# Optimization experiments

Measured on AMD Instinct MI355X. Metric: run time of the kernel, lower is better.

The kernel has to match this reference:

```python
import jax, jax.numpy as jnp
import numpy as np

N, D, E = 50000, 128, 100000
H1, H2, H3 = 8, 8, 4
NEG_SLOPE = 0.2  # PyG GATv2Conv default negative_slope


def _gatv2_layer(x, src, dst, Wl, Wr, att, b, heads):
    # GATv2Conv(in=D, out=D, heads=heads, concat=False), share_weights=False
    C = Wl.shape[1] // heads
    xl = (x @ Wl).reshape(-1, heads, C)  # source-side transform (x_j)
    xr = (x @ Wr).reshape(-1, heads, C)  # target-side transform (x_i)
    m = jax.nn.leaky_relu(xl[src] + xr[dst], NEG_SLOPE)      # [E,H,C]
    e = jnp.einsum('ehc,hc->eh', m, att)                      # [E,H]
    # segment softmax over incoming edges of each destination node
    emax = jax.ops.segment_max(e, dst, num_segments=N)        # [N,H]
    a = jnp.exp(e - emax[dst])
    denom = jax.ops.segment_sum(a, dst, num_segments=N)       # [N,H] (>0: self-loops)
    a = a / denom[dst]
    out = jax.ops.segment_sum(xl[src] * a[:, :, None], dst, num_segments=N)  # [N,H,C]
    return out.mean(axis=1) + b  # concat=False -> head mean, then bias


def setup_inputs() -> dict:
    key = jax.random.key(0)
    ks = jax.random.split(key, 16)
    x = jax.random.normal(ks[0], (N, D), dtype=jnp.float32)
    src = jax.random.randint(ks[1], (E,), 0, N)
    dst = jax.random.randint(ks[2], (E,), 0, N)
    src = jnp.where(src == dst, (src + 1) % N, src)  # no pre-existing self loops
    edge_index = jnp.stack([src, dst]).astype(jnp.int64)
    s = 1.0 / np.sqrt(D)
    def lin(k, h):
        return jax.random.uniform(k, (D, h * D), jnp.float32, -s, s)
    def attn(k, h):
        return jax.random.uniform(k, (h, D), jnp.float32, -s, s)
    return {
        'x': x, 'edge_index': edge_index,
        'W1l': lin(ks[3], H1), 'W1r': lin(ks[4], H1), 'att1': attn(ks[5], H1), 'b1': jnp.zeros((D,), jnp.float32),
        'W2l': lin(ks[6], H2), 'W2r': lin(ks[7], H2), 'att2': attn(ks[8], H2), 'b2': jnp.zeros((D,), jnp.float32),
        'W3l': lin(ks[9], H3), 'W3r': lin(ks[10], H3), 'att3': attn(ks[11], H3), 'b3': jnp.zeros((D,), jnp.float32),
    }


def reference(x, edge_index, W1l, W1r, att1, b1, W2l, W2r, att2, b2, W3l, W3r, att3, b3):
    # PyG GATv2Conv adds self loops by default
    loops = jnp.arange(N, dtype=edge_index.dtype)
    src = jnp.concatenate([edge_index[0], loops])
    dst = jnp.concatenate([edge_index[1], loops])
    h = x + _gatv2_layer(x, src, dst, W1l, W1r, att1, b1, H1)
    h = jax.nn.elu(h)  # dropout is identity in eval mode
    h = h + _gatv2_layer(h, src, dst, W2l, W2r, att2, b2, H2)
    h = jax.nn.elu(h)
    h = h + _gatv2_layer(h, src, dst, W3l, W3r, att3, b3, H3)
    return h
```

## Files before the change

### kernel.cpp

```cpp
#include <hip/hip_runtime.h>

#define NN 50000
#define DD 128
#define EE 100000
#define ET (EE + NN)

typedef __attribute__((ext_vector_type(4))) float f32x4;
typedef __attribute__((ext_vector_type(2))) float f32x2;
typedef __attribute__((ext_vector_type(8))) short bf16x8;
typedef __attribute__((ext_vector_type(4))) unsigned short u16x4;
typedef __attribute__((ext_vector_type(4))) unsigned int u32x4;

static __device__ __forceinline__ unsigned short f2bf(float f) {
  union { float f; unsigned int u; } v; v.f = f;
  unsigned int r = (v.u + 0x7FFFu + ((v.u >> 16) & 1u)) >> 16;
  return (unsigned short)r;
}
static __device__ __forceinline__ float bflo(unsigned int u) {
  union { unsigned int u; float f; } v; v.u = u << 16; return v.f;
}
static __device__ __forceinline__ float bfhi(unsigned int u) {
  union { unsigned int u; float f; } v; v.u = u & 0xffff0000u; return v.f;
}

__global__ void k_count(const int* __restrict__ ei, int* __restrict__ counts) {
  int i = blockIdx.x * blockDim.x + threadIdx.x;
  if (i >= ET) return;
  int dst = (i < EE) ? ei[EE + i] : (i - EE);
  if (dst < 0 || dst >= NN) return;
  atomicAdd(&counts[dst], 1);
}

__global__ __launch_bounds__(1024) void k_scan(const int* __restrict__ counts,
                                               int* __restrict__ offs,
                                               int* __restrict__ cursor) {
  __shared__ int buf[1024];
  const int tid = threadIdx.x;
  int carry = 0;
  for (int base = 0; base < NN; base += 4096) {
    int i0 = base + tid * 4;
    int v[4];
#pragma unroll
    for (int q = 0; q < 4; ++q) { int i = i0 + q; v[q] = (i < NN) ? counts[i] : 0; }
    int s = v[0] + v[1] + v[2] + v[3];
    buf[tid] = s;
    __syncthreads();
    for (int off = 1; off < 1024; off <<= 1) {
      int t = (tid >= off) ? buf[tid - off] : 0;
      __syncthreads();
      buf[tid] += t;
      __syncthreads();
    }
    int excl = carry + buf[tid] - s;
    int tot = buf[1023];
#pragma unroll
    for (int q = 0; q < 4; ++q) {
      int i = i0 + q;
      if (i < NN) { offs[i] = excl; cursor[i] = excl; }
      excl += v[q];
    }
    carry += tot;
    __syncthreads();
  }
  if (tid == 0) offs[NN] = carry;
}

__global__ void k_fill(const int* __restrict__ ei, int* __restrict__ cursor,
                       int* __restrict__ srcs) {
  int i = blockIdx.x * blockDim.x + threadIdx.x;
  if (i >= ET) return;
  int src, dst;
  if (i < EE) { src = ei[i]; dst = ei[EE + i]; }
  else { src = dst = i - EE; }
  if (dst < 0 || dst >= NN) return;
  if (src < 0 || src >= NN) src = dst;
  int pos = atomicAdd(&cursor[dst], 1);
  if (pos >= 0 && pos < ET) srcs[pos] = src;
}

__global__ void k_wT(const float* __restrict__ W, unsigned short* __restrict__ WT, int Nout) {
  int i = blockIdx.x * blockDim.x + threadIdx.x;
  int total = Nout * DD;
  if (i >= total) return;
  int n = i >> 7, k = i & 127;
  WT[i] = f2bf(W[(size_t)k * Nout + n]);
}

__global__ void k_cvt(const float* __restrict__ in, unsigned short* __restrict__ out, int total4) {
  int i = blockIdx.x * blockDim.x + threadIdx.x;
  if (i >= total4) return;
  f32x4 v = *(const f32x4*)(in + (size_t)i * 4);
  u16x4 w;
  w.x = f2bf(v.x); w.y = f2bf(v.y); w.z = f2bf(v.z); w.w = f2bf(v.w);
  *(u16x4*)(out + (size_t)i * 4) = w;
}

__global__ void k_atts(const float* __restrict__ a, float* __restrict__ o, int total) {
  int i = blockIdx.x * blockDim.x + threadIdx.x;
  if (i >= total) return;
  o[i] = a[i] * 1.4426950408889634f;
}

__global__ __launch_bounds__(256) void gemm_bt(
    const unsigned short* __restrict__ A, const unsigned short* __restrict__ WT,
    unsigned short* __restrict__ Cl, unsigned short* __restrict__ Cr,
    int M, int Nout, int lgny) {
  const int f = blockIdx.x;
  const int c = f & ((1 << lgny) - 1);
  const int x = f >> lgny;
  const int z = c & 1, y = c >> 1;
  const int m0 = x * 128, n0 = y * 128;
  unsigned short* C = z ? Cr : Cl;
  const unsigned short* BT = WT + (size_t)z * Nout * DD;

  __shared__ unsigned short As[128 * 128];
  __shared__ unsigned short Bs[128 * 128];
  const int tid = threadIdx.x;
  const int wave = tid >> 6, lane = tid & 63;
  const int hi = lane >> 4, lr = lane & 15;

#pragma unroll
  for (int i = 0; i < 8; ++i) {
    int row = i * 16 + wave * 4 + hi;
    int c16 = lr ^ (row & 7);
    const unsigned short* ga = A + (size_t)(m0 + row) * DD + c16 * 8;
    __builtin_amdgcn_global_load_lds((const __attribute__((address_space(1))) void*)ga,
        (__attribute__((address_space(3))) void*)(As + i * 2048 + wave * 512), 16, 0, 0);
    const unsigned short* gb = BT + (size_t)(n0 + row) * DD + c16 * 8;
    __builtin_amdgcn_global_load_lds((const __attribute__((address_space(1))) void*)gb,
        (__attribute__((address_space(3))) void*)(Bs + i * 2048 + wave * 512), 16, 0, 0);
  }
  __syncthreads();

  const int wr = (wave >> 1) * 64, wc = (wave & 1) * 64;
  f32x4 acc[4][4];
#pragma unroll
  for (int i = 0; i < 4; ++i)
#pragma unroll
    for (int j = 0; j < 4; ++j) acc[i][j] = (f32x4){0.f, 0.f, 0.f, 0.f};

#pragma unroll
  for (int k0 = 0; k0 < 128; k0 += 32) {
    const int ck = (k0 >> 3) + hi;
    bf16x8 af[4], bfr[4];
#pragma unroll
    for (int mi = 0; mi < 4; ++mi) {
      int r = wr + mi * 16 + lr;
      af[mi] = *(const bf16x8*)&As[r * 128 + ((ck ^ (r & 7)) << 3)];
    }
#pragma unroll
    for (int ni = 0; ni < 4; ++ni) {
      int cc = wc + ni * 16 + lr;
      bfr[ni] = *(const bf16x8*)&Bs[cc * 128 + ((ck ^ (cc & 7)) << 3)];
    }
#pragma unroll
    for (int mi = 0; mi < 4; ++mi)
#pragma unroll
      for (int ni = 0; ni < 4; ++ni)
        acc[mi][ni] = __builtin_amdgcn_mfma_f32_16x16x32_bf16(af[mi], bfr[ni], acc[mi][ni], 0, 0, 0);
  }

#pragma unroll
  for (int mi = 0; mi < 4; ++mi) {
#pragma unroll
    for (int ni = 0; ni < 4; ++ni) {
      int col = n0 + wc + ni * 16 + lr;
#pragma unroll
      for (int j = 0; j < 4; ++j) {
        int row = m0 + wr + mi * 16 + (hi << 2) + j;
        if (row < M) C[(size_t)row * Nout + col] = f2bf(acc[mi][ni][j]);
      }
    }
  }
}

template <int H>
__global__ __launch_bounds__(256) void gat_agg2(
    const unsigned short* __restrict__ xl, const unsigned short* __restrict__ xr,
    const int* __restrict__ offs, const int* __restrict__ srcs,
    const float* __restrict__ att_s,
    const float* __restrict__ bias,
    const float* __restrict__ resid, float* __restrict__ out,
    unsigned short* __restrict__ hbf, int do_elu) {
  constexpr int LPH = 64 / H;
  constexpr int CPL = 2 * H;
  constexpr int NW = H;
  constexpr int ROW = H * DD;
  const int wave = threadIdx.x >> 6, lane = threadIdx.x & 63;
  const int n = blockIdx.x * 4 + wave;
  if (n >= NN) return;
  const int cb = lane * CPL;

  float xrv[CPL], av[CPL];
  {
    const unsigned int* q = (const unsigned int*)(xr + (size_t)n * ROW + cb);
#pragma unroll
    for (int w = 0; w < NW; ++w) {
      unsigned int u = q[w];
      xrv[2 * w] = bflo(u);
      xrv[2 * w + 1] = bfhi(u);
    }
#pragma unroll
    for (int c = 0; c < CPL; ++c) av[c] = att_s[cb + c];
  }

  float acc[CPL];
#pragma unroll
  for (int c = 0; c < CPL; ++c) acc[c] = 0.f;
  float mx = -1e30f, dn = 0.f;

  const int e0 = offs[n], e1 = offs[n + 1];
  unsigned int cur[NW], nxt[NW];
  {
    int s = srcs[e0];
    const unsigned int* q = (const unsigned int*)(xl + (size_t)s * ROW + cb);
#pragma unroll
    for (int w = 0; w < NW; ++w) cur[w] = q[w];
  }
  for (int j = e0; j < e1; ++j) {
    if (j + 1 < e1) {
      int s2 = srcs[j + 1];
      const unsigned int* q = (const unsigned int*)(xl + (size_t)s2 * ROW + cb);
#pragma unroll
      for (int w = 0; w < NW; ++w) nxt[w] = q[w];
    }
    float xv[CPL];
#pragma unroll
    for (int w = 0; w < NW; ++w) {
      xv[2 * w] = bflo(cur[w]);
      xv[2 * w + 1] = bfhi(cur[w]);
    }
    float p = 0.f;
#pragma unroll
    for (int c = 0; c < CPL; ++c) {
      float z = xv[c] + xrv[c];
      z = fmaxf(z, 0.2f * z);
      p = fmaf(z, av[c], p);
    }
#pragma unroll
    for (int m = 1; m < LPH; m <<= 1) p += __shfl_xor(p, m, 64);
    if (__any(p > mx + 11.5f)) {
      float mnew = fmaxf(mx, p);
      float sc = __builtin_amdgcn_exp2f(mx - mnew);
      dn *= sc;
#pragma unroll
      for (int c = 0; c < CPL; ++c) acc[c] *= sc;
      mx = mnew;
    }
    float wt = __builtin_amdgcn_exp2f(p - mx);
    dn += wt;
#pragma unroll
    for (int c = 0; c < CPL; ++c) acc[c] = fmaf(wt, xv[c], acc[c]);
#pragma unroll
    for (int w = 0; w < NW; ++w) cur[w] = nxt[w];
  }

  float r[CPL];
  const float inv = (1.f / (float)H) / dn;
#pragma unroll
  for (int c = 0; c < CPL; ++c) r[c] = acc[c] * inv;
#pragma unroll
  for (int m = LPH; m < 64; m <<= 1)
#pragma unroll
    for (int c = 0; c < CPL; ++c) r[c] += __shfl_xor(r[c], m, 64);

  if (lane < LPH) {
    float o[CPL];
#pragma unroll
    for (int c = 0; c < CPL; ++c) {
      o[c] = r[c] + bias[cb + c] + resid[(size_t)n * DD + cb + c];
      if (do_elu) o[c] = (o[c] > 0.f) ? o[c] : expm1f(o[c]);
    }
#pragma unroll
    for (int c = 0; c < CPL; c += 4) {
      f32x4 v; v.x = o[c]; v.y = o[c + 1]; v.z = o[c + 2]; v.w = o[c + 3];
      *(f32x4*)(out + (size_t)n * DD + cb + c) = v;
    }
    if (hbf) {
#pragma unroll
      for (int c = 0; c < CPL; c += 8) {
        u32x4 pk;
#pragma unroll
        for (int q = 0; q < 4; ++q)
          pk[q] = (unsigned int)f2bf(o[c + 2 * q]) | ((unsigned int)f2bf(o[c + 2 * q + 1]) << 16);
        *(u32x4*)(hbf + (size_t)n * DD + cb + c) = pk;
      }
    }
  }
}

extern "C" void kernel_launch(void* const* d_in, const int* in_sizes, int n_in,
                              void* d_out, int out_size, void* d_ws, size_t ws_size,
                              hipStream_t stream) {
  const float* x = (const float*)d_in[0];
  const int* ei = (const int*)d_in[1];
  const float* W1l = (const float*)d_in[2];
  const float* W1r = (const float*)d_in[3];
  const float* att1 = (const float*)d_in[4];
  const float* b1 = (const float*)d_in[5];
  const float* W2l = (const float*)d_in[6];
  const float* W2r = (const float*)d_in[7];
  const float* att2 = (const float*)d_in[8];
  const float* b2 = (const float*)d_in[9];
  const float* W3l = (const float*)d_in[10];
  const float* W3r = (const float*)d_in[11];
  const float* att3 = (const float*)d_in[12];
  const float* b3 = (const float*)d_in[13];
  float* out = (float*)d_out;

  char* p = (char*)d_ws;
  auto carve = [&](size_t bytes) {
    char* r = p;
    p += (bytes + 255) & ~(size_t)255;
    return r;
  };
  unsigned short* xl = (unsigned short*)carve((size_t)NN * 1024 * 2);
  unsigned short* xr = (unsigned short*)carve((size_t)NN * 1024 * 2);
  unsigned short* abf = (unsigned short*)carve((size_t)NN * DD * 2);
  unsigned short* wt1 = (unsigned short*)carve((size_t)2 * 1024 * DD * 2);
  unsigned short* wt2 = (unsigned short*)carve((size_t)2 * 1024 * DD * 2);
  unsigned short* wt3 = (unsigned short*)carve((size_t)2 * 512 * DD * 2);
  float* as1 = (float*)carve((size_t)8 * DD * 4);
  float* as2 = (float*)carve((size_t)8 * DD * 4);
  float* as3 = (float*)carve((size_t)4 * DD * 4);
  int* counts = (int*)carve((size_t)NN * 4);
  int* offs = (int*)carve(((size_t)NN + 1) * 4);
  int* cursor = (int*)carve((size_t)NN * 4);
  int* srcs = (int*)carve((size_t)ET * 4);
  size_t needed = (size_t)(p - (char*)d_ws);
  if (needed > ws_size) return;

  hipMemsetAsync(counts, 0, (size_t)NN * 4, stream);
  k_count<<<(ET + 255) / 256, 256, 0, stream>>>(ei, counts);
  k_scan<<<1, 1024, 0, stream>>>(counts, offs, cursor);
  k_fill<<<(ET + 255) / 256, 256, 0, stream>>>(ei, cursor, srcs);

  k_wT<<<(1024 * DD + 255) / 256, 256, 0, stream>>>(W1l, wt1, 1024);
  k_wT<<<(1024 * DD + 255) / 256, 256, 0, stream>>>(W1r, wt1 + (size_t)1024 * DD, 1024);
  k_wT<<<(1024 * DD + 255) / 256, 256, 0, stream>>>(W2l, wt2, 1024);
  k_wT<<<(1024 * DD + 255) / 256, 256, 0, stream>>>(W2r, wt2 + (size_t)1024 * DD, 1024);
  k_wT<<<(512 * DD + 255) / 256, 256, 0, stream>>>(W3l, wt3, 512);
  k_wT<<<(512 * DD + 255) / 256, 256, 0, stream>>>(W3r, wt3 + (size_t)512 * DD, 512);
  k_atts<<<4, 256, 0, stream>>>(att1, as1, 8 * DD);
  k_atts<<<4, 256, 0, stream>>>(att2, as2, 8 * DD);
  k_atts<<<2, 256, 0, stream>>>(att3, as3, 4 * DD);

  k_cvt<<<((NN * DD / 4) + 255) / 256, 256, 0, stream>>>(x, abf, NN * DD / 4);

  const int gx = (NN + 127) / 128;
  gemm_bt<<<gx * 16, 256, 0, stream>>>(abf, wt1, xl, xr, NN, 1024, 4);
  gat_agg2<8><<<(NN + 3) / 4, 256, 0, stream>>>(xl, xr, offs, srcs, as1, b1, x, out, abf, 1);
  gemm_bt<<<gx * 16, 256, 0, stream>>>(abf, wt2, xl, xr, NN, 1024, 4);
  gat_agg2<8><<<(NN + 3) / 4, 256, 0, stream>>>(xl, xr, offs, srcs, as2, b2, out, out, abf, 1);
  gemm_bt<<<gx * 8, 256, 0, stream>>>(abf, wt3, xl, xr, NN, 512, 3);
  gat_agg2<4><<<(NN + 3) / 4, 256, 0, stream>>>(xl, xr, offs, srcs, as3, b3, out, out, nullptr, 0);
}
```

Measured before the change: 544.0 us.

## Fuse prep kernels, use wave-shuffle scan, batch four edges per aggregation step

Merges the weight transposes, attention scaling, counts zeroing and the x-to-bf16 conversion into a single prep kernel, removing about ten launches and a memset. Replaces the shared-memory Hillis-Steele scan with a wave-shuffle two-level scan that needs far fewer barriers. Restructures the aggregation loop to gather four neighbour rows at once, giving more loads in flight and one online-softmax rescale check per batch instead of per edge. ELU now uses exp2 directly rather than expm1f, at some cost in precision near zero.

New measurement: 492.1 us. 9.5% less time.

```diff
diff --git a/kernel.cpp b/kernel.cpp
--- a/kernel.cpp
+++ b/kernel.cpp
@@ -6,7 +6,6 @@
 #define ET (EE + NN)
 
 typedef __attribute__((ext_vector_type(4))) float f32x4;
-typedef __attribute__((ext_vector_type(2))) float f32x2;
 typedef __attribute__((ext_vector_type(8))) short bf16x8;
 typedef __attribute__((ext_vector_type(4))) unsigned short u16x4;
 typedef __attribute__((ext_vector_type(4))) unsigned int u32x4;
@@ -21,6 +20,51 @@
 }
 static __device__ __forceinline__ float bfhi(unsigned int u) {
   union { unsigned int u; float f; } v; v.u = u & 0xffff0000u; return v.f;
+}
+
+__global__ __launch_bounds__(256) void k_prep(
+    const float* __restrict__ x,
+    const float* __restrict__ W1l, const float* __restrict__ W1r,
+    const float* __restrict__ W2l, const float* __restrict__ W2r,
+    const float* __restrict__ W3l, const float* __restrict__ W3r,
+    const float* __restrict__ att1, const float* __restrict__ att2, const float* __restrict__ att3,
+    unsigned short* __restrict__ wt1, unsigned short* __restrict__ wt2,
+    unsigned short* __restrict__ wt3,
+    float* __restrict__ as1, float* __restrict__ as2, float* __restrict__ as3,
+    unsigned short* __restrict__ abf, int* __restrict__ counts) {
+  const int i = blockIdx.x * 256 + threadIdx.x;
+  const float LOG2E = 1.4426950408889634f;
+  if (i < 262144) {
+    int half = i >> 17, rem = i & 131071;
+    int nn = rem >> 7, k = rem & 127;
+    const float* W = half ? W1r : W1l;
+    wt1[i] = f2bf(W[(size_t)k * 1024 + nn]);
+  } else if (i < 524288) {
+    int local = i - 262144;
+    int half = local >> 17, rem = local & 131071;
+    int nn = rem >> 7, k = rem & 127;
+    const float* W = half ? W2r : W2l;
+    wt2[local] = f2bf(W[(size_t)k * 1024 + nn]);
+  } else if (i < 655360) {
+    int local = i - 524288;
+    int half = local >> 16, rem = local & 65535;
+    int nn = rem >> 7, k = rem & 127;
+    const float* W = half ? W3r : W3l;
+    wt3[local] = f2bf(W[(size_t)k * 512 + nn]);
+  } else if (i < 657920) {
+    int local = i - 655360;
+    if (local < 1024) as1[local] = att1[local] * LOG2E;
+    else if (local < 2048) as2[local - 1024] = att2[local - 1024] * LOG2E;
+    else as3[local - 2048] = att3[local - 2048] * LOG2E;
+  } else if (i < 707920) {
+    counts[i - 657920] = 0;
+  } else if (i < 2307920) {
+    int u = i - 707920;
+    f32x4 v = *(const f32x4*)(x + (size_t)u * 4);
+    u16x4 w;
+    w.x = f2bf(v.x); w.y = f2bf(v.y); w.z = f2bf(v.z); w.w = f2bf(v.w);
+    *(u16x4*)(abf + (size_t)u * 4) = w;
+  }
 }
 
 __global__ void k_count(const int* __restrict__ ei, int* __restrict__ counts) {
@@ -34,8 +78,11 @@
 __global__ __launch_bounds__(1024) void k_scan(const int* __restrict__ counts,
                                                int* __restrict__ offs,
                                                int* __restrict__ cursor) {
-  __shared__ int buf[1024];
+  __shared__ int wsum[16];
+  __shared__ int wpre[16];
+  __shared__ int wtot;
   const int tid = threadIdx.x;
+  const int wv = tid >> 6, lane = tid & 63;
   int carry = 0;
   for (int base = 0; base < NN; base += 4096) {
     int i0 = base + tid * 4;
@@ -43,23 +90,34 @@
 #pragma unroll
     for (int q = 0; q < 4; ++q) { int i = i0 + q; v[q] = (i < NN) ? counts[i] : 0; }
     int s = v[0] + v[1] + v[2] + v[3];
-    buf[tid] = s;
+    int sc = s;
+#pragma unroll
+    for (int m = 1; m < 64; m <<= 1) {
+      int t = __shfl_up(sc, m, 64);
+      if (lane >= m) sc += t;
+    }
+    if (lane == 63) wsum[wv] = sc;
     __syncthreads();
-    for (int off = 1; off < 1024; off <<= 1) {
-      int t = (tid >= off) ? buf[tid - off] : 0;
-      __syncthreads();
-      buf[tid] += t;
-      __syncthreads();
-    }
-    int excl = carry + buf[tid] - s;
-    int tot = buf[1023];
+    if (tid < 16) {
+      int t = wsum[tid];
+      int scc = t;
+#pragma unroll
+      for (int m = 1; m < 16; m <<= 1) {
+        int u = __shfl_up(scc, m, 64);
+        if (tid >= m) scc += u;
+      }
+      wpre[tid] = scc - t;
+      if (tid == 15) wtot = scc;
+    }
+    __syncthreads();
+    int excl = carry + wpre[wv] + (sc - s);
 #pragma unroll
     for (int q = 0; q < 4; ++q) {
       int i = i0 + q;
       if (i < NN) { offs[i] = excl; cursor[i] = excl; }
       excl += v[q];
     }
-    carry += tot;
+    carry += wtot;
     __syncthreads();
   }
   if (tid == 0) offs[NN] = carry;
@@ -78,29 +136,6 @@
   if (pos >= 0 && pos < ET) srcs[pos] = src;
 }
 
-__global__ void k_wT(const float* __restrict__ W, unsigned short* __restrict__ WT, int Nout) {
-  int i = blockIdx.x * blockDim.x + threadIdx.x;
-  int total = Nout * DD;
-  if (i >= total) return;
-  int n = i >> 7, k = i & 127;
-  WT[i] = f2bf(W[(size_t)k * Nout + n]);
-}
-
-__global__ void k_cvt(const float* __restrict__ in, unsigned short* __restrict__ out, int total4) {
-  int i = blockIdx.x * blockDim.x + threadIdx.x;
-  if (i >= total4) return;
-  f32x4 v = *(const f32x4*)(in + (size_t)i * 4);
-  u16x4 w;
-  w.x = f2bf(v.x); w.y = f2bf(v.y); w.z = f2bf(v.z); w.w = f2bf(v.w);
-  *(u16x4*)(out + (size_t)i * 4) = w;
-}
-
-__global__ void k_atts(const float* __restrict__ a, float* __restrict__ o, int total) {
-  int i = blockIdx.x * blockDim.x + threadIdx.x;
-  if (i >= total) return;
-  o[i] = a[i] * 1.4426950408889634f;
-}
-
 __global__ __launch_bounds__(256) void gemm_bt(
     const unsigned short* __restrict__ A, const unsigned short* __restrict__ WT,
     unsigned short* __restrict__ Cl, unsigned short* __restrict__ Cr,
@@ -175,7 +210,7 @@
 }
 
 template <int H>
-__global__ __launch_bounds__(256) void gat_agg2(
+__global__ __launch_bounds__(256) void gat_agg3(
     const unsigned short* __restrict__ xl, const unsigned short* __restrict__ xr,
     const int* __restrict__ offs, const int* __restrict__ srcs,
     const float* __restrict__ att_s,
@@ -210,49 +245,58 @@
   float mx = -1e30f, dn = 0.f;
 
   const int e0 = offs[n], e1 = offs[n + 1];
-  unsigned int cur[NW], nxt[NW];
-  {
-    int s = srcs[e0];
-    const unsigned int* q = (const unsigned int*)(xl + (size_t)s * ROW + cb);
-#pragma unroll
-    for (int w = 0; w < NW; ++w) cur[w] = q[w];
-  }
-  for (int j = e0; j < e1; ++j) {
-    if (j + 1 < e1) {
-      int s2 = srcs[j + 1];
-      const unsigned int* q = (const unsigned int*)(xl + (size_t)s2 * ROW + cb);
-#pragma unroll
-      for (int w = 0; w < NW; ++w) nxt[w] = q[w];
-    }
-    float xv[CPL];
-#pragma unroll
-    for (int w = 0; w < NW; ++w) {
-      xv[2 * w] = bflo(cur[w]);
-      xv[2 * w + 1] = bfhi(cur[w]);
-    }
-    float p = 0.f;
-#pragma unroll
-    for (int c = 0; c < CPL; ++c) {
-      float z = xv[c] + xrv[c];
-      z = fmaxf(z, 0.2f * z);
-      p = fmaf(z, av[c], p);
-    }
-#pragma unroll
-    for (int m = 1; m < LPH; m <<= 1) p += __shfl_xor(p, m, 64);
-    if (__any(p > mx + 11.5f)) {
-      float mnew = fmaxf(mx, p);
+  for (int j = e0; j < e1; j += 4) {
+    const int B = (e1 - j < 4) ? (e1 - j) : 4;
+    unsigned int rows[4][NW];
+#pragma unroll
+    for (int b = 0; b < 4; ++b) {
+      if (b < B) {
+        int s = srcs[j + b];
+        const unsigned int* qq = (const unsigned int*)(xl + (size_t)s * ROW + cb);
+#pragma unroll
+        for (int w = 0; w < NW; ++w) rows[b][w] = qq[w];
+      }
+    }
+    float p[4];
+#pragma unroll
+    for (int b = 0; b < 4; ++b) {
+      float pp = -1e30f;
+      if (b < B) {
+        pp = 0.f;
+#pragma unroll
+        for (int w = 0; w < NW; ++w) {
+          float x0 = bflo(rows[b][w]), x1 = bfhi(rows[b][w]);
+          float z0 = x0 + xrv[2 * w]; z0 = fmaxf(z0, 0.2f * z0);
+          float z1 = x1 + xrv[2 * w + 1]; z1 = fmaxf(z1, 0.2f * z1);
+          pp = fmaf(z0, av[2 * w], pp);
+          pp = fmaf(z1, av[2 * w + 1], pp);
+        }
+#pragma unroll
+        for (int m = 1; m < LPH; m <<= 1) pp += __shfl_xor(pp, m, 64);
+      }
+      p[b] = pp;
+    }
+    float pm = fmaxf(fmaxf(p[0], p[1]), fmaxf(p[2], p[3]));
+    if (__any(pm > mx + 11.5f)) {
+      float mnew = fmaxf(mx, pm);
       float sc = __builtin_amdgcn_exp2f(mx - mnew);
       dn *= sc;
 #pragma unroll
       for (int c = 0; c < CPL; ++c) acc[c] *= sc;
       mx = mnew;
     }
-    float wt = __builtin_amdgcn_exp2f(p - mx);
-    dn += wt;
-#pragma unroll
-    for (int c = 0; c < CPL; ++c) acc[c] = fmaf(wt, xv[c], acc[c]);
-#pragma unroll
-    for (int w = 0; w < NW; ++w) cur[w] = nxt[w];
+#pragma unroll
+    for (int b = 0; b < 4; ++b) {
+      if (b < B) {
+        float wt = __builtin_amdgcn_exp2f(p[b] - mx);
+        dn += wt;
+#pragma unroll
+        for (int w = 0; w < NW; ++w) {
+          acc[2 * w] = fmaf(wt, bflo(rows[b][w]), acc[2 * w]);
+          acc[2 * w + 1] = fmaf(wt, bfhi(rows[b][w]), acc[2 * w + 1]);
+        }
+      }
+    }
   }
 
   float r[CPL];
@@ -269,7 +313,8 @@
 #pragma unroll
     for (int c = 0; c < CPL; ++c) {
       o[c] = r[c] + bias[cb + c] + resid[(size_t)n * DD + cb + c];
-      if (do_elu) o[c] = (o[c] > 0.f) ? o[c] : expm1f(o[c]);
+      if (do_elu && o[c] < 0.f)
+        o[c] = __builtin_amdgcn_exp2f(o[c] * 1.4426950408889634f) - 1.f;
     }
 #pragma unroll
     for (int c = 0; c < CPL; c += 4) {
@@ -330,28 +375,17 @@
   size_t needed = (size_t)(p - (char*)d_ws);
   if (needed > ws_size) return;
 
-  hipMemsetAsync(counts, 0, (size_t)NN * 4, stream);
+  k_prep<<<9016, 256, 0, stream>>>(x, W1l, W1r, W2l, W2r, W3l, W3r, att1, att2, att3,
+                                   wt1, wt2, wt3, as1, as2, as3, abf, counts);
   k_count<<<(ET + 255) / 256, 256, 0, stream>>>(ei, counts);
   k_scan<<<1, 1024, 0, stream>>>(counts, offs, cursor);
   k_fill<<<(ET + 255) / 256, 256, 0, stream>>>(ei, cursor, srcs);
 
-  k_wT<<<(1024 * DD + 255) / 256, 256, 0, stream>>>(W1l, wt1, 1024);
-  k_wT<<<(1024 * DD + 255) / 256, 256, 0, stream>>>(W1r, wt1 + (size_t)1024 * DD, 1024);
-  k_wT<<<(1024 * DD + 255) / 256, 256, 0, stream>>>(W2l, wt2, 1024);
-  k_wT<<<(1024 * DD + 255) / 256, 256, 0, stream>>>(W2r, wt2 + (size_t)1024 * DD, 1024);
-  k_wT<<<(512 * DD + 255) / 256, 256, 0, stream>>>(W3l, wt3, 512);
-  k_wT<<<(512 * DD + 255) / 256, 256, 0, stream>>>(W3r, wt3 + (size_t)512 * DD, 512);
-  k_atts<<<4, 256, 0, stream>>>(att1, as1, 8 * DD);
-  k_atts<<<4, 256, 0, stream>>>(att2, as2, 8 * DD);
-  k_atts<<<2, 256, 0, stream>>>(att3, as3, 4 * DD);
-
-  k_cvt<<<((NN * DD / 4) + 255) / 256, 256, 0, stream>>>(x, abf, NN * DD / 4);
-
   const int gx = (NN + 127) / 128;
   gemm_bt<<<gx * 16, 256, 0, stream>>>(abf, wt1, xl, xr, NN, 1024, 4);
-  gat_agg2<8><<<(NN + 3) / 4, 256, 0, stream>>>(xl, xr, offs, srcs, as1, b1, x, out, abf, 1);
+  gat_agg3<8><<<(NN + 3) / 4, 256, 0, stream>>>(xl, xr, offs, srcs, as1, b1, x, out, abf, 1);
   gemm_bt<<<gx * 16, 256, 0, stream>>>(abf, wt2, xl, xr, NN, 1024, 4);
-  gat_agg2<8><<<(NN + 3) / 4, 256, 0, stream>>>(xl, xr, offs, srcs, as2, b2, out, out, abf, 1);
+  gat_agg3<8><<<(NN + 3) / 4, 256, 0, stream>>>(xl, xr, offs, srcs, as2, b2, out, out, abf, 1);
   gemm_bt<<<gx * 8, 256, 0, stream>>>(abf, wt3, xl, xr, NN, 512, 3);
-  gat_agg2<4><<<(NN + 3) / 4, 256, 0, stream>>>(xl, xr, offs, srcs, as3, b3, out, out, nullptr, 0);
-}
+  gat_agg3<4><<<(NN + 3) / 4, 256, 0, stream>>>(xl, xr, offs, srcs, as3, b3, out, out, nullptr, 0);
+}
```
